# Performance work log

Measured on AMD Instinct MI355X. Metric: run time of the kernel, lower is better.

The kernel has to match this reference:

```python
import jax, jax.numpy as jnp
import numpy as np

D, H, NL, DFF, VS, VT = 512, 8, 6, 2048, 32000, 32000
B, SS, ST = 4, 512, 512
PAD = 1
EPS = 1e-5


def _pos_encoding(S, d):
    pos = jnp.arange(S, dtype=jnp.float32)[:, None]
    div = jnp.exp(jnp.arange(0, d, 2, dtype=jnp.float32) * (-jnp.log(jnp.float32(10000.0)) / d))
    pe = jnp.zeros((S, d), dtype=jnp.float32)
    pe = pe.at[:, 0::2].set(jnp.sin(pos * div))
    pe = pe.at[:, 1::2].set(jnp.cos(pos * div))
    return pe


def _ln(x, g, b):
    m = jnp.mean(x, axis=-1, keepdims=True)
    v = jnp.mean(jnp.square(x - m), axis=-1, keepdims=True)
    return (x - m) * jax.lax.rsqrt(v + EPS) * g + b


def _mha(q, k, v, Wq, Wk, Wv, Wo, mask):
    # q,k,v: [B,S,D]; W*: [D,D] (torch Linear: y = x @ W.T); mask True -> masked
    Bq, Sq, _ = q.shape
    Sk = k.shape[1]
    dk = D // H
    Q = (q @ Wq.T).reshape(Bq, Sq, H, dk).transpose(0, 2, 1, 3)
    K = (k @ Wk.T).reshape(Bq, Sk, H, dk).transpose(0, 2, 1, 3)
    V = (v @ Wv.T).reshape(Bq, Sk, H, dk).transpose(0, 2, 1, 3)
    scores = jnp.einsum('bhqd,bhkd->bhqk', Q, K) / jnp.sqrt(jnp.float32(dk))
    scores = jnp.where(mask, -jnp.inf, scores)
    w = jax.nn.softmax(scores, axis=-1)
    w = jnp.nan_to_num(w)  # matches torch.nan_to_num after softmax of all -inf rows
    out = jnp.einsum('bhqk,bhkd->bhqd', w, V)
    out = out.transpose(0, 2, 1, 3).reshape(Bq, Sq, D)
    return out @ Wo.T


def _ffn(x, w1, b1, w2, b2):
    return jax.nn.relu(x @ w1.T + b1) @ w2.T + b2


def setup_inputs() -> dict:
    key = jax.random.key(0)
    ks = jax.random.split(key, 48)
    i = iter(range(48))
    n = lambda shape, s=0.02: jax.random.normal(ks[next(i)], shape, dtype=jnp.float32) * s
    inp = {
        'src': jax.random.randint(ks[next(i)], (B, SS), 0, VS),
        'tgt': jax.random.randint(ks[next(i)], (B, ST), 0, VT),
        'src_embed': n((VS, D)),
        'tgt_embed': n((VT, D)),
        'enc_Wq': n((NL, D, D)), 'enc_Wk': n((NL, D, D)), 'enc_Wv': n((NL, D, D)), 'enc_Wo': n((NL, D, D)),
        'enc_w1': n((NL, DFF, D)), 'enc_b1': jnp.zeros((NL, DFF)),
        'enc_w2': n((NL, D, DFF)), 'enc_b2': jnp.zeros((NL, D)),
        'enc_ln1g': jnp.ones((NL, D)), 'enc_ln1b': jnp.zeros((NL, D)),
        'enc_ln2g': jnp.ones((NL, D)), 'enc_ln2b': jnp.zeros((NL, D)),
        'enc_lnfg': jnp.ones((D,)), 'enc_lnfb': jnp.zeros((D,)),
        'dec_sWq': n((NL, D, D)), 'dec_sWk': n((NL, D, D)), 'dec_sWv': n((NL, D, D)), 'dec_sWo': n((NL, D, D)),
        'dec_cWq': n((NL, D, D)), 'dec_cWk': n((NL, D, D)), 'dec_cWv': n((NL, D, D)), 'dec_cWo': n((NL, D, D)),
        'dec_w1': n((NL, DFF, D)), 'dec_b1': jnp.zeros((NL, DFF)),
        'dec_w2': n((NL, D, DFF)), 'dec_b2': jnp.zeros((NL, D)),
        'dec_ln1g': jnp.ones((NL, D)), 'dec_ln1b': jnp.zeros((NL, D)),
        'dec_ln2g': jnp.ones((NL, D)), 'dec_ln2b': jnp.zeros((NL, D)),
        'dec_ln3g': jnp.ones((NL, D)), 'dec_ln3b': jnp.zeros((NL, D)),
        'dec_lnfg': jnp.ones((D,)), 'dec_lnfb': jnp.zeros((D,)),
        'out_W': n((VT, D)), 'out_b': jnp.zeros((VT,)),
    }
    return inp


def reference(src, tgt, src_embed, tgt_embed,
              enc_Wq, enc_Wk, enc_Wv, enc_Wo, enc_w1, enc_b1, enc_w2, enc_b2,
              enc_ln1g, enc_ln1b, enc_ln2g, enc_ln2b, enc_lnfg, enc_lnfb,
              dec_sWq, dec_sWk, dec_sWv, dec_sWo, dec_cWq, dec_cWk, dec_cWv, dec_cWo,
              dec_w1, dec_b1, dec_w2, dec_b2,
              dec_ln1g, dec_ln1b, dec_ln2g, dec_ln2b, dec_ln3g, dec_ln3b,
              dec_lnfg, dec_lnfb, out_W, out_b):
    scale = jnp.sqrt(jnp.float32(D))
    src_mask = (src == PAD)[:, None, None, :]                      # [B,1,1,SS]
    causal = jnp.triu(jnp.ones((ST, ST), dtype=bool), k=1)[None, None]
    tgt_mask = (tgt == PAD)[:, None, None, :] | causal             # [B,1,ST,ST]

    # Encoder
    x = src_embed[src] * scale + _pos_encoding(SS, D)[None]
    for l in range(NL):
        nrm = _ln(x, enc_ln1g[l], enc_ln1b[l])
        x = x + _mha(nrm, nrm, nrm, enc_Wq[l], enc_Wk[l], enc_Wv[l], enc_Wo[l], src_mask)
        x = x + _ffn(_ln(x, enc_ln2g[l], enc_ln2b[l]), enc_w1[l], enc_b1[l], enc_w2[l], enc_b2[l])
    memory = _ln(x, enc_lnfg, enc_lnfb)

    # Decoder
    y = tgt_embed[tgt] * scale + _pos_encoding(ST, D)[None]
    for l in range(NL):
        nrm = _ln(y, dec_ln1g[l], dec_ln1b[l])
        y = y + _mha(nrm, nrm, nrm, dec_sWq[l], dec_sWk[l], dec_sWv[l], dec_sWo[l], tgt_mask)
        nrm = _ln(y, dec_ln2g[l], dec_ln2b[l])
        y = y + _mha(nrm, memory, memory, dec_cWq[l], dec_cWk[l], dec_cWv[l], dec_cWo[l], src_mask)
        y = y + _ffn(_ln(y, dec_ln3g[l], dec_ln3b[l]), dec_w1[l], dec_b1[l], dec_w2[l], dec_b2[l])
    y = _ln(y, dec_lnfg, dec_lnfb)

    logits = y @ out_W.T + out_b                                   # [B,ST,VT]
    return logits
```

## Files before the change

kernel.cpp:

```cpp
#include <hip/hip_runtime.h>
#include <hip/hip_bf16.h>
#include <math.h>

#define Dm    512
#define Hh    8
#define NLay  6
#define DFFm  2048
#define Bb    4
#define NTOK  2048
#define PADID 1
#define LNEPS 1e-5f
#define S2W   262144

typedef __attribute__((ext_vector_type(8))) short short8;
typedef __attribute__((ext_vector_type(4))) float f32x4;
typedef unsigned short u16;

__device__ __forceinline__ u16 f2bf(float f) {
    union { float f; unsigned int i; } x; x.f = f;
    unsigned int r = x.i + 0x7fffu + ((x.i >> 16) & 1u);
    return (u16)(r >> 16);
}

typedef const __attribute__((address_space(1))) void* as1cv;
typedef __attribute__((address_space(3))) void* as3v;
__device__ __forceinline__ void gl_lds16(const u16* g, u16* l) {
    __builtin_amdgcn_global_load_lds((as1cv)g, (as3v)l, 16, 0, 0);
}

#define SYNC_VM(N) do { \
    asm volatile("s_waitcnt vmcnt(" #N ")" ::: "memory"); \
    __builtin_amdgcn_s_barrier(); \
    __builtin_amdgcn_sched_barrier(0); \
} while (0)

__device__ __forceinline__ void swz_tile(int& mt, int& nt) {
    const int nwg  = gridDim.x * gridDim.y;
    const int orig = blockIdx.y * gridDim.x + blockIdx.x;
    const int q8 = nwg >> 3, r8 = nwg & 7;
    const int xcd = orig & 7, idx = orig >> 3;
    const int wgid = (xcd < r8 ? xcd * (q8 + 1) : r8 * (q8 + 1) + (xcd - r8) * q8) + idx;
    const int MT = gridDim.y;
    mt = wgid % MT;
    nt = wgid / MT;
}

struct CvtJobs {
    const float* s[17];
    u16*         d[17];
    long         n4[17];
};
__global__ __launch_bounds__(256) void cvt_many(CvtJobs j) {
    const int job = blockIdx.y;
    const long n4 = j.n4[job];
    const float* in = j.s[job];
    u16* out = j.d[job];
    long i = (long)blockIdx.x * 256 + threadIdx.x;
    const long stride = (long)gridDim.x * 256;
    for (; i < n4; i += stride) {
        float4 v = ((const float4*)in)[i];
        ushort4 o;
        o.x = f2bf(v.x); o.y = f2bf(v.y); o.z = f2bf(v.z); o.w = f2bf(v.w);
        ((ushort4*)out)[i] = o;
    }
}

__global__ __launch_bounds__(256) void gemm_bt(
    const u16* __restrict__ A0, const u16* __restrict__ A1,
    const u16* __restrict__ A2, int lda,
    const u16* __restrict__ B0, const u16* __restrict__ B1,
    const u16* __restrict__ B2, int ldb,
    float* Cf, u16* Cb, int csm,
    const float* __restrict__ bias, int relu,
    int Kc, int ns, int vth, int koff, u16* vtp)
{
    __shared__ u16 As[2][4096];
    __shared__ u16 Bs[2][4096];
    int mt, nt; swz_tile(mt, nt);
    const int m0 = mt << 6, n0 = nt << 6;
    const int t = threadIdx.x, lane = t & 63, wave = t >> 6;
    const int wr = (wave >> 1) << 5, wc = (wave & 1) << 5;
    const int fr = lane & 15, fq = lane >> 4;
    const int srow = t >> 3;
    const int sch  = (t & 7) ^ (srow & 7);

    const int p = n0 >> 9;
    const u16* Amat = (p == 0) ? A0 : (p == 1 ? A1 : A2);
    const u16* Bmat; int nb;
    if (B1) { Bmat = (p == 0) ? B0 : (p == 1 ? B1 : B2); nb = n0 & 511; }
    else    { Bmat = B0; nb = n0; }
    const long kb = (long)blockIdx.z * Kc;

    const u16* Ag0 = Amat + (long)(m0 + srow) * lda + kb + (sch << 3);
    const u16* Ag1 = Ag0 + 32L * lda;
    const u16* Bg0 = Bmat + (long)(nb + srow) * ldb + kb + (sch << 3);
    const u16* Bg1 = Bg0 + 32L * ldb;

    f32x4 acc[2][2];
    #pragma unroll
    for (int i = 0; i < 2; i++)
        #pragma unroll
        for (int j = 0; j < 2; j++) acc[i][j] = (f32x4){0.f, 0.f, 0.f, 0.f};

    const int nk = Kc >> 6;
    gl_lds16(Ag0, &As[0][t << 3]);
    gl_lds16(Ag1, &As[0][(t + 256) << 3]);
    gl_lds16(Bg0, &Bs[0][t << 3]);
    gl_lds16(Bg1, &Bs[0][(t + 256) << 3]);
    __syncthreads();
    for (int ki = 0; ki < nk; ki++) {
        const int cur = ki & 1;
        if (ki + 1 < nk) {
            const int ko = (ki + 1) << 6;
            gl_lds16(Ag0 + ko, &As[cur ^ 1][t << 3]);
            gl_lds16(Ag1 + ko, &As[cur ^ 1][(t + 256) << 3]);
            gl_lds16(Bg0 + ko, &Bs[cur ^ 1][t << 3]);
            gl_lds16(Bg1 + ko, &Bs[cur ^ 1][(t + 256) << 3]);
        }
        const int r0 = wr + fr, r1 = wr + 16 + fr;
        const int c0 = wc + fr, c1 = wc + 16 + fr;
        #pragma unroll
        for (int h = 0; h < 2; h++) {
            const int lc = fq | (h << 2);
            short8 af0 = *(const short8*)&As[cur][(r0 << 6) + ((lc ^ (r0 & 7)) << 3)];
            short8 af1 = *(const short8*)&As[cur][(r1 << 6) + ((lc ^ (r1 & 7)) << 3)];
            short8 bf0 = *(const short8*)&Bs[cur][(c0 << 6) + ((lc ^ (c0 & 7)) << 3)];
            short8 bf1 = *(const short8*)&Bs[cur][(c1 << 6) + ((lc ^ (c1 & 7)) << 3)];
            acc[0][0] = __builtin_amdgcn_mfma_f32_16x16x32_bf16(af0, bf0, acc[0][0], 0, 0, 0);
            acc[0][1] = __builtin_amdgcn_mfma_f32_16x16x32_bf16(af0, bf1, acc[0][1], 0, 0, 0);
            acc[1][0] = __builtin_amdgcn_mfma_f32_16x16x32_bf16(af1, bf0, acc[1][0], 0, 0, 0);
            acc[1][1] = __builtin_amdgcn_mfma_f32_16x16x32_bf16(af1, bf1, acc[1][1], 0, 0, 0);
        }
        __syncthreads();
    }

    #pragma unroll
    for (int i = 0; i < 2; i++) {
        #pragma unroll
        for (int j = 0; j < 2; j++) {
            const int nl  = n0 + wc + (j << 4) + fr;
            const int mlb = m0 + wr + (i << 4) + (fq << 2);
            const float bsv = bias ? bias[nl] : 0.f;
            #pragma unroll
            for (int r = 0; r < 4; r++) {
                const int ml = mlb + r;
                if (ns > 1) {
                    float v = acc[i][j][r] + (blockIdx.z == 0 ? bsv : 0.f);
                    unsafeAtomicAdd(&Cf[(long)ml * csm + nl + koff], v);
                } else {
                    float v = acc[i][j][r] + bsv;
                    if (nl >= vth) {
                        vtp[(long)(ml >> 9) * S2W + (long)(nl - vth) * 512 + (ml & 511)] = f2bf(v);
                    } else {
                        if (relu) v = fmaxf(v, 0.f);
                        long ci = (long)ml * csm + nl + koff;
                        if (Cf) Cf[ci] = v;
                        if (Cb) Cb[ci] = f2bf(v);
                    }
                }
            }
        }
    }
}

__global__ __launch_bounds__(256) void gemm_kv6(
    const u16* __restrict__ A,
    const u16* __restrict__ Wk, const u16* __restrict__ Wv,
    u16* __restrict__ kc, u16* __restrict__ vtc)
{
    __shared__ u16 As[2][4096];
    __shared__ u16 Bs[2][4096];
    int mt, nt; swz_tile(mt, nt);
    const int m0 = mt << 6, n0 = nt << 6;
    const int z = blockIdx.z;
    const int t = threadIdx.x, lane = t & 63, wave = t >> 6;
    const int wr = (wave >> 1) << 5, wc = (wave & 1) << 5;
    const int fr = lane & 15, fq = lane >> 4;
    const int srow = t >> 3;
    const int sch  = (t & 7) ^ (srow & 7);

    const int p = n0 >> 9;
    const u16* Bmat = ((p == 0) ? Wk : Wv) + (size_t)z * S2W;
    const int nb = n0 & 511;

    const u16* Ag0 = A + (long)(m0 + srow) * 512 + (sch << 3);
    const u16* Ag1 = Ag0 + 32L * 512;
    const u16* Bg0 = Bmat + (long)(nb + srow) * 512 + (sch << 3);
    const u16* Bg1 = Bg0 + 32L * 512;

    f32x4 acc[2][2];
    #pragma unroll
    for (int i = 0; i < 2; i++)
        #pragma unroll
        for (int j = 0; j < 2; j++) acc[i][j] = (f32x4){0.f, 0.f, 0.f, 0.f};

    gl_lds16(Ag0, &As[0][t << 3]);
    gl_lds16(Ag1, &As[0][(t + 256) << 3]);
    gl_lds16(Bg0, &Bs[0][t << 3]);
    gl_lds16(Bg1, &Bs[0][(t + 256) << 3]);
    __syncthreads();
    for (int ki = 0; ki < 8; ki++) {
        const int cur = ki & 1;
        if (ki + 1 < 8) {
            const int ko = (ki + 1) << 6;
            gl_lds16(Ag0 + ko, &As[cur ^ 1][t << 3]);
            gl_lds16(Ag1 + ko, &As[cur ^ 1][(t + 256) << 3]);
            gl_lds16(Bg0 + ko, &Bs[cur ^ 1][t << 3]);
            gl_lds16(Bg1 + ko, &Bs[cur ^ 1][(t + 256) << 3]);
        }
        const int r0 = wr + fr, r1 = wr + 16 + fr;
        const int c0 = wc + fr, c1 = wc + 16 + fr;
        #pragma unroll
        for (int h = 0; h < 2; h++) {
            const int lc = fq | (h << 2);
            short8 af0 = *(const short8*)&As[cur][(r0 << 6) + ((lc ^ (r0 & 7)) << 3)];
            short8 af1 = *(const short8*)&As[cur][(r1 << 6) + ((lc ^ (r1 & 7)) << 3)];
            short8 bf0 = *(const short8*)&Bs[cur][(c0 << 6) + ((lc ^ (c0 & 7)) << 3)];
            short8 bf1 = *(const short8*)&Bs[cur][(c1 << 6) + ((lc ^ (c1 & 7)) << 3)];
            acc[0][0] = __builtin_amdgcn_mfma_f32_16x16x32_bf16(af0, bf0, acc[0][0], 0, 0, 0);
            acc[0][1] = __builtin_amdgcn_mfma_f32_16x16x32_bf16(af0, bf1, acc[0][1], 0, 0, 0);
            acc[1][0] = __builtin_amdgcn_mfma_f32_16x16x32_bf16(af1, bf0, acc[1][0], 0, 0, 0);
            acc[1][1] = __builtin_amdgcn_mfma_f32_16x16x32_bf16(af1, bf1, acc[1][1], 0, 0, 0);
        }
        __syncthreads();
    }

    #pragma unroll
    for (int i = 0; i < 2; i++) {
        #pragma unroll
        for (int j = 0; j < 2; j++) {
            const int nl  = n0 + wc + (j << 4) + fr;
            const int mlb = m0 + wr + (i << 4) + (fq << 2);
            #pragma unroll
            for (int r = 0; r < 4; r++) {
                const int ml = mlb + r;
                const u16 v = f2bf(acc[i][j][r]);
                if (nl < 512)
                    kc[(long)z * NTOK * 512 + (long)ml * 512 + nl] = v;
                else
                    vtc[(long)z * Bb * S2W + (long)(ml >> 9) * S2W +
                        (long)(nl - 512) * 512 + (ml & 511)] = v;
            }
        }
    }
}

__global__ __launch_bounds__(256) void gemm_big(
    const u16* __restrict__ A, int lda,
    const u16* __restrict__ B, int ldb,
    float* Cf, int ldc,
    const float* __restrict__ bias, int K)
{
    __shared__ u16 As[3][4096];
    __shared__ u16 Bs[3][4096];
    int mt, nt; swz_tile(mt, nt);
    const int m0 = mt << 7, n0 = nt << 7;
    const int t = threadIdx.x, lane = t & 63, wave = t >> 6;
    const int wr = (wave >> 1) << 6, wc = (wave & 1) << 6;
    const int fr = lane & 15, fq = lane >> 4;
    const int srow = t >> 2;
    const int sch  = (t & 3) ^ ((srow >> 1) & 3);
    const u16* Ag0 = A + (long)(m0 + srow) * lda + (sch << 3);
    const u16* Ag1 = A + (long)(m0 + 64 + srow) * lda + (sch << 3);
    const u16* Bg0 = B + (long)(n0 + srow) * ldb + (sch << 3);
    const u16* Bg1 = B + (long)(n0 + 64 + srow) * ldb + (sch << 3);

    f32x4 acc[4][4];
    #pragma unroll
    for (int i = 0; i < 4; i++)
        #pragma unroll
        for (int j = 0; j < 4; j++) acc[i][j] = (f32x4){0.f, 0.f, 0.f, 0.f};

    const int nk = K >> 5;
    auto stage = [&](int ki, int buf) {
        const int ko = ki << 5;
        gl_lds16(Ag0 + ko, &As[buf][t << 3]);
        gl_lds16(Ag1 + ko, &As[buf][(t + 256) << 3]);
        gl_lds16(Bg0 + ko, &Bs[buf][t << 3]);
        gl_lds16(Bg1 + ko, &Bs[buf][(t + 256) << 3]);
    };
    stage(0, 0);
    if (nk > 1) { stage(1, 1); SYNC_VM(4); }
    else        { SYNC_VM(0); }

    int cur = 0;
    for (int ki = 0; ki < nk; ki++) {
        const bool st = (ki + 2 < nk);
        if (st) stage(ki + 2, cur == 0 ? 2 : cur - 1);
        short8 af[4], bf[4];
        #pragma unroll
        for (int i = 0; i < 4; i++) {
            const int r = wr + (i << 4) + fr;
            af[i] = *(const short8*)&As[cur][(r << 5) + ((fq ^ ((r >> 1) & 3)) << 3)];
        }
        #pragma unroll
        for (int j = 0; j < 4; j++) {
            const int c = wc + (j << 4) + fr;
            bf[j] = *(const short8*)&Bs[cur][(c << 5) + ((fq ^ ((c >> 1) & 3)) << 3)];
        }
        #pragma unroll
        for (int i = 0; i < 4; i++)
            #pragma unroll
            for (int j = 0; j < 4; j++)
                acc[i][j] = __builtin_amdgcn_mfma_f32_16x16x32_bf16(af[i], bf[j], acc[i][j], 0, 0, 0);
        if (ki + 1 < nk) {
            if (st) SYNC_VM(4);
            else    SYNC_VM(0);
        }
        cur = (cur == 2) ? 0 : cur + 1;
    }

    #pragma unroll
    for (int i = 0; i < 4; i++) {
        #pragma unroll
        for (int j = 0; j < 4; j++) {
            const int nl  = n0 + wc + (j << 4) + fr;
            const int mlb = m0 + wr + (i << 4) + (fq << 2);
            const float bsv = bias ? bias[nl] : 0.f;
            #pragma unroll
            for (int r = 0; r < 4; r++)
                Cf[(long)(mlb + r) * ldc + nl] = acc[i][j][r] + bsv;
        }
    }
}

__global__ __launch_bounds__(256) void attn_fused(
    const u16* __restrict__ qkb, const u16* __restrict__ kb_, int ldk,
    const u16* __restrict__ vt,
    const int* __restrict__ ids, u16* __restrict__ attc, int causal)
{
    __shared__ u16 Ks[2][4096];
    __shared__ u16 Vs[2][4096];
    __shared__ short Ps[4][16][72];
    const int t = threadIdx.x, lane = t & 63, w = t >> 6;
    const int fr = lane & 15, fq = lane >> 4;
    const int qh = w & 1, kvh = w >> 1;
    const int q0 = blockIdx.x << 5, h = blockIdx.y, b = blockIdx.z;

    const u16* qp = qkb + (long)(b * 512 + q0 + (qh << 4) + fr) * 1024 + h * 64 + (fq << 3);
    short8 aq0 = *(const short8*)qp;
    short8 aq1 = *(const short8*)(qp + 32);

    const int sr = t >> 3, sc = (t & 7) ^ (sr & 7);
    const u16* kg0 = kb_ + (long)(b * 512 + sr) * ldk + h * 64 + (sc << 3);
    const u16* kg1 = kg0 + 32L * ldk;
    const u16* vg0 = vt + (long)b * S2W + (long)(h * 64 + sr) * 512 + (sc << 3);
    const u16* vg1 = vg0 + 32L * 512;

    unsigned pmask = 0;
    #pragma unroll
    for (int kt = 0; kt < 8; kt++)
        #pragma unroll
        for (int j = 0; j < 4; j++)
            if (ids[b * 512 + (kt << 6) + (j << 4) + fr] == PADID)
                pmask |= 1u << ((kt << 2) + j);

    const int nkt = causal ? (((q0 + 31) >> 6) + 1) : 8;
    const int nA = (nkt + 1) >> 1, nB = nkt - nA;
    const int myn = kvh ? nB : nA;

    float m[4], l[4]; f32x4 oc[4];
    #pragma unroll
    for (int r = 0; r < 4; r++) { m[r] = -INFINITY; l[r] = 0.f; oc[r] = (f32x4){0.f,0.f,0.f,0.f}; }

    for (int i = 0; i < nA; i++) {
        {
            const long soA = (long)(i << 6);
            gl_lds16(kg0 + soA * ldk, &Ks[0][t << 3]);
            gl_lds16(kg1 + soA * ldk, &Ks[0][(t + 256) << 3]);
            gl_lds16(vg0 + soA,       &Vs[0][t << 3]);
            gl_lds16(vg1 + soA,       &Vs[0][(t + 256) << 3]);
            if (i < nB) {
                const long soB = (long)((nA + i) << 6);
                gl_lds16(kg0 + soB * ldk, &Ks[1][t << 3]);
                gl_lds16(kg1 + soB * ldk, &Ks[1][(t + 256) << 3]);
                gl_lds16(vg0 + soB,       &Vs[1][t << 3]);
                gl_lds16(vg1 + soB,       &Vs[1][(t + 256) << 3]);
            }
        }
        __syncthreads();

        if (i < myn) {
            const int kt = (kvh ? nA : 0) + i;
            f32x4 sc4[4];
            #pragma unroll
            for (int j = 0; j < 4; j++) sc4[j] = (f32x4){0.f,0.f,0.f,0.f};
            #pragma unroll
            for (int j = 0; j < 4; j++) {
                const int rr = (j << 4) + fr;
                short8 bk0 = *(const short8*)&Ks[kvh][rr * 64 + ((fq ^ (rr & 7)) << 3)];
                short8 bk1 = *(const short8*)&Ks[kvh][rr * 64 + (((fq | 4) ^ (rr & 7)) << 3)];
                sc4[j] = __builtin_amdgcn_mfma_f32_16x16x32_bf16(aq0, bk0, sc4[j], 0, 0, 0);
                sc4[j] = __builtin_amdgcn_mfma_f32_16x16x32_bf16(aq1, bk1, sc4[j], 0, 0, 0);
            }
            const int s0 = kt << 6;
            #pragma unroll
            for (int r = 0; r < 4; r++) {
                const int qa = q0 + (qh << 4) + (fq << 2) + r;
                float mx = -INFINITY;
                #pragma unroll
                for (int j = 0; j < 4; j++) {
                    bool msk = ((pmask >> ((kt << 2) + j)) & 1) ||
                               (causal && (s0 + (j << 4) + fr) > qa);
                    float sv = msk ? -INFINITY : sc4[j][r] * 0.125f;
                    sc4[j][r] = sv;
                    mx = fmaxf(mx, sv);
                }
                mx = fmaxf(mx, __shfl_xor(mx, 1)); mx = fmaxf(mx, __shfl_xor(mx, 2));
                mx = fmaxf(mx, __shfl_xor(mx, 4)); mx = fmaxf(mx, __shfl_xor(mx, 8));
                float mnew  = fmaxf(m[r], mx);
                float scale = (mnew == -INFINITY) ? 1.f : __expf(m[r] - mnew);
                float ps = 0.f;
                #pragma unroll
                for (int j = 0; j < 4; j++) {
                    float p2 = (sc4[j][r] == -INFINITY) ? 0.f : __expf(sc4[j][r] - mnew);
                    sc4[j][r] = p2; ps += p2;
                }
                ps += __shfl_xor(ps, 1); ps += __shfl_xor(ps, 2);
                ps += __shfl_xor(ps, 4); ps += __shfl_xor(ps, 8);
                l[r] = l[r] * scale + ps;
                m[r] = mnew;
                #pragma unroll
                for (int j2 = 0; j2 < 4; j2++) oc[j2][r] *= scale;
            }
            #pragma unroll
            for (int r = 0; r < 4; r++)
                #pragma unroll
                for (int j = 0; j < 4; j++)
                    Ps[w][(fq << 2) + r][(j << 4) + fr] = (short)f2bf(sc4[j][r]);
            #pragma unroll
            for (int kc2 = 0; kc2 < 2; kc2++) {
                short8 pa = *(const short8*)&Ps[w][fr][(kc2 << 5) + (fq << 3)];
                #pragma unroll
                for (int j2 = 0; j2 < 4; j2++) {
                    const int rd = (j2 << 4) + fr;
                    const int cch = (((kc2 << 2) | fq) ^ (rd & 7));
                    short8 bv = *(const short8*)&Vs[kvh][rd * 64 + (cch << 3)];
                    oc[j2] = __builtin_amdgcn_mfma_f32_16x16x32_bf16(pa, bv, oc[j2], 0, 0, 0);
                }
            }
        }
        __syncthreads();
    }

    float* Ob = (float*)&Ks[0][0];
    float* Ml = (float*)&Vs[0][0];
    if (kvh == 1) {
        #pragma unroll
        for (int r = 0; r < 4; r++) {
            const int row = (qh << 4) + (fq << 2) + r;
            Ml[(row << 1)]     = m[r];
            Ml[(row << 1) + 1] = l[r];
            #pragma unroll
            for (int j2 = 0; j2 < 4; j2++)
                Ob[(row << 6) + (j2 << 4) + fr] = oc[j2][r];
        }
    }
    __syncthreads();
    if (kvh == 0) {
        #pragma unroll
        for (int r = 0; r < 4; r++) {
            const int row = (qh << 4) + (fq << 2) + r;
            const float mB = Ml[(row << 1)], lB = Ml[(row << 1) + 1];
            const float mN = fmaxf(m[r], mB);
            float sA, sB;
            if (mN == -INFINITY) { sA = 0.f; sB = 0.f; }
            else {
                sA = (m[r] == -INFINITY) ? 0.f : __expf(m[r] - mN);
                sB = (mB   == -INFINITY) ? 0.f : __expf(mB   - mN);
            }
            const float L = l[r] * sA + lB * sB;
            const float inv = (L > 0.f) ? 1.f / L : 0.f;
            #pragma unroll
            for (int j2 = 0; j2 < 4; j2++) {
                float val = (oc[j2][r] * sA + Ob[(row << 6) + (j2 << 4) + fr] * sB) * inv;
                attc[(long)(b * 512 + q0 + (qh << 4) + (fq << 2) + r) * 512 +
                     h * 64 + (j2 << 4) + fr] = f2bf(val);
            }
        }
    }
}

__global__ __launch_bounds__(256) void ln_rows(
    const float* __restrict__ x, const float* __restrict__ g,
    const float* __restrict__ b, u16* __restrict__ out)
{
    int row  = blockIdx.x * 4 + (threadIdx.x >> 6);
    int lane = threadIdx.x & 63;
    const float* xr = x + (long)row * Dm;
    float v[8]; float s = 0.f;
    #pragma unroll
    for (int i = 0; i < 8; i++) { v[i] = xr[lane + (i << 6)]; s += v[i]; }
    #pragma unroll
    for (int o = 32; o > 0; o >>= 1) s += __shfl_xor(s, o);
    float mean = s * (1.f / 512.f);
    float q = 0.f;
    #pragma unroll
    for (int i = 0; i < 8; i++) { float d = v[i] - mean; q += d * d; }
    #pragma unroll
    for (int o = 32; o > 0; o >>= 1) q += __shfl_xor(q, o);
    float rinv = rsqrtf(q * (1.f / 512.f) + LNEPS);
    u16* orow = out + (long)row * Dm;
    #pragma unroll
    for (int i = 0; i < 8; i++) {
        int c = lane + (i << 6);
        orow[c] = f2bf((v[i] - mean) * rinv * g[c] + b[c]);
    }
}

__global__ __launch_bounds__(256) void embed_pe(
    const int* __restrict__ ids, const float* __restrict__ emb,
    float* __restrict__ out)
{
    int idx = blockIdx.x * 256 + threadIdx.x;
    int d   = idx & 511;
    int tok = idx >> 9;
    int s   = tok & 511;
    int id  = ids[tok];
    float val = emb[(long)id * Dm + d] * 22.62741699796952f;
    int i2 = d >> 1;
    float dv  = expf((float)(i2 << 1) * (-9.210340371976184f / 512.f));
    float ang = (float)s * dv;
    val += (d & 1) ? cosf(ang) : sinf(ang);
    out[idx] = val;
}

extern "C" void kernel_launch(void* const* d_in, const int* in_sizes, int n_in,
                              void* d_out, int out_size, void* d_ws, size_t ws_size,
                              hipStream_t stream)
{
    (void)in_sizes; (void)n_in; (void)out_size; (void)ws_size;
    const int*   src       = (const int*)d_in[0];
    const int*   tgt       = (const int*)d_in[1];
    const float* src_embed = (const float*)d_in[2];
    const float* tgt_embed = (const float*)d_in[3];
    const float* enc_b1  = (const float*)d_in[9];
    const float* enc_b2  = (const float*)d_in[11];
    const float* enc_ln1g = (const float*)d_in[12];
    const float* enc_ln1b = (const float*)d_in[13];
    const float* enc_ln2g = (const float*)d_in[14];
    const float* enc_ln2b = (const float*)d_in[15];
    const float* enc_lnfg = (const float*)d_in[16];
    const float* enc_lnfb = (const float*)d_in[17];
    const float* dec_b1  = (const float*)d_in[27];
    const float* dec_b2  = (const float*)d_in[29];
    const float* dec_ln1g = (const float*)d_in[30];
    const float* dec_ln1b = (const float*)d_in[31];
    const float* dec_ln2g = (const float*)d_in[32];
    const float* dec_ln2b = (const float*)d_in[33];
    const float* dec_ln3g = (const float*)d_in[34];
    const float* dec_ln3b = (const float*)d_in[35];
    const float* dec_lnfg = (const float*)d_in[36];
    const float* dec_lnfb = (const float*)d_in[37];
    const float* out_b  = (const float*)d_in[39];

    char* wp = (char*)d_ws;
    auto carve = [&](size_t nbytes) {
        void* p = (void*)wp; wp += (nbytes + 255) & ~(size_t)255; return p;
    };

    const long nW = (long)NLay * S2W;
    const long nF = (long)NLay * DFFm * Dm;
    const long nO = 32000L * Dm;

    u16* Wb[12];
    for (int i = 0; i < 12; i++) Wb[i] = (u16*)carve((size_t)nW * 2);
    u16* w1E  = (u16*)carve((size_t)nF * 2);
    u16* w2E  = (u16*)carve((size_t)nF * 2);
    u16* w1D  = (u16*)carve((size_t)nF * 2);
    u16* w2D  = (u16*)carve((size_t)nF * 2);
    u16* outW = (u16*)carve((size_t)nO * 2);

    float* x  = (float*)carve((size_t)NTOK * Dm * 4);
    float* y  = (float*)carve((size_t)NTOK * Dm * 4);
    u16* nrm  = (u16*)carve((size_t)NTOK * Dm * 2);
    u16* qkb  = (u16*)carve((size_t)NTOK * 1024 * 2);
    u16* vt   = (u16*)carve((size_t)Bb * Dm * 512 * 2);
    u16* attc = (u16*)carve((size_t)NTOK * Dm * 2);
    u16* h1   = (u16*)carve((size_t)NTOK * DFFm * 2);
    u16* memn = (u16*)carve((size_t)NTOK * Dm * 2);
    u16* kc6  = (u16*)carve((size_t)NLay * NTOK * 512 * 2);
    u16* vt6  = (u16*)carve((size_t)NLay * Bb * S2W * 2);

    const int wi[12] = {4, 5, 6, 7, 18, 19, 20, 21, 22, 23, 24, 25};
    CvtJobs jobs;
    for (int i = 0; i < 12; i++) {
        jobs.s[i] = (const float*)d_in[wi[i]]; jobs.d[i] = Wb[i]; jobs.n4[i] = nW >> 2;
    }
    jobs.s[12] = (const float*)d_in[8];  jobs.d[12] = w1E;  jobs.n4[12] = nF >> 2;
    jobs.s[13] = (const float*)d_in[10]; jobs.d[13] = w2E;  jobs.n4[13] = nF >> 2;
    jobs.s[14] = (const float*)d_in[26]; jobs.d[14] = w1D;  jobs.n4[14] = nF >> 2;
    jobs.s[15] = (const float*)d_in[28]; jobs.d[15] = w2D;  jobs.n4[15] = nF >> 2;
    jobs.s[16] = (const float*)d_in[38]; jobs.d[16] = outW; jobs.n4[16] = nO >> 2;
    cvt_many<<<dim3(512, 17), 256, 0, stream>>>(jobs);

    const int BIG = 1 << 28;
    u16 *eWq = Wb[0], *eWk = Wb[1], *eWv = Wb[2], *eWo = Wb[3];
    u16 *sWq = Wb[4], *sWk = Wb[5], *sWv = Wb[6], *sWo = Wb[7];
    u16 *cWq = Wb[8], *cWk = Wb[9], *cWv = Wb[10], *cWo = Wb[11];

    embed_pe<<<4096, 256, 0, stream>>>(src, src_embed, x);
    for (int l = 0; l < NLay; l++) {
        const size_t wo = (size_t)l * S2W;
        ln_rows<<<512, 256, 0, stream>>>(x, enc_ln1g + l * Dm, enc_ln1b + l * Dm, nrm);
        gemm_bt<<<dim3(24, 32, 1), 256, 0, stream>>>(nrm, nrm, nrm, 512,
            eWq + wo, eWk + wo, eWv + wo, 512,
            nullptr, qkb, 1024, nullptr, 0, 512, 1, 1024, 0, vt);
        attn_fused<<<dim3(16, Hh, Bb), 256, 0, stream>>>(qkb, qkb + 512, 1024, vt, src, attc, 0);
        gemm_bt<<<dim3(8, 32, 2), 256, 0, stream>>>(attc, attc, attc, 512,
            eWo + wo, nullptr, nullptr, 512,
            x, nullptr, 512, nullptr, 0, 256, 2, BIG, 0, nullptr);
        ln_rows<<<512, 256, 0, stream>>>(x, enc_ln2g + l * Dm, enc_ln2b + l * Dm, nrm);
        gemm_bt<<<dim3(32, 32, 1), 256, 0, stream>>>(nrm, nrm, nrm, 512,
            w1E + (size_t)l * DFFm * Dm, nullptr, nullptr, 512,
            nullptr, h1, DFFm, enc_b1 + l * DFFm, 1, 512, 1, BIG, 0, nullptr);
        gemm_bt<<<dim3(8, 32, 4), 256, 0, stream>>>(h1, h1, h1, DFFm,
            w2E + (size_t)l * Dm * DFFm, nullptr, nullptr, DFFm,
            x, nullptr, 512, enc_b2 + l * Dm, 0, 512, 4, BIG, 0, nullptr);
    }
    ln_rows<<<512, 256, 0, stream>>>(x, enc_lnfg, enc_lnfb, memn);
    gemm_kv6<<<dim3(16, 32, NLay), 256, 0, stream>>>(memn, cWk, cWv, kc6, vt6);

    embed_pe<<<4096, 256, 0, stream>>>(tgt, tgt_embed, y);
    for (int l = 0; l < NLay; l++) {
        const size_t wo = (size_t)l * S2W;
        ln_rows<<<512, 256, 0, stream>>>(y, dec_ln1g + l * Dm, dec_ln1b + l * Dm, nrm);
        gemm_bt<<<dim3(24, 32, 1), 256, 0, stream>>>(nrm, nrm, nrm, 512,
            sWq + wo, sWk + wo, sWv + wo, 512,
            nullptr, qkb, 1024, nullptr, 0, 512, 1, 1024, 0, vt);
        attn_fused<<<dim3(16, Hh, Bb), 256, 0, stream>>>(qkb, qkb + 512, 1024, vt, tgt, attc, 1);
        gemm_bt<<<dim3(8, 32, 2), 256, 0, stream>>>(attc, attc, attc, 512,
            sWo + wo, nullptr, nullptr, 512,
            y, nullptr, 512, nullptr, 0, 256, 2, BIG, 0, nullptr);
        ln_rows<<<512, 256, 0, stream>>>(y, dec_ln2g + l * Dm, dec_ln2b + l * Dm, nrm);
        gemm_bt<<<dim3(8, 32, 1), 256, 0, stream>>>(nrm, nrm, nrm, 512,
            cWq + wo, nullptr, nullptr, 512,
            nullptr, qkb, 1024, nullptr, 0, 512, 1, BIG, 0, nullptr);
        attn_fused<<<dim3(16, Hh, Bb), 256, 0, stream>>>(qkb,
            kc6 + (size_t)l * NTOK * 512, 512, vt6 + (size_t)l * Bb * S2W, src, attc, 0);
        gemm_bt<<<dim3(8, 32, 2), 256, 0, stream>>>(attc, attc, attc, 512,
            cWo + wo, nullptr, nullptr, 512,
            y, nullptr, 512, nullptr, 0, 256, 2, BIG, 0, nullptr);
        ln_rows<<<512, 256, 0, stream>>>(y, dec_ln3g + l * Dm, dec_ln3b + l * Dm, nrm);
        gemm_bt<<<dim3(32, 32, 1), 256, 0, stream>>>(nrm, nrm, nrm, 512,
            w1D + (size_t)l * DFFm * Dm, nullptr, nullptr, 512,
            nullptr, h1, DFFm, dec_b1 + l * DFFm, 1, 512, 1, BIG, 0, nullptr);
        gemm_bt<<<dim3(8, 32, 4), 256, 0, stream>>>(h1, h1, h1, DFFm,
            w2D + (size_t)l * Dm * DFFm, nullptr, nullptr, DFFm,
            y, nullptr, 512, dec_b2 + l * Dm, 0, 512, 4, BIG, 0, nullptr);
    }
    ln_rows<<<512, 256, 0, stream>>>(y, dec_lnfg, dec_lnfb, nrm);

    gemm_big<<<dim3(250, 16), 256, 0, stream>>>(nrm, 512, outW, 512,
        (float*)d_out, 32000, out_b, 512);
}
```

Before: 1.570 ms.

## Switch GEMM mainloops to 3-stage LDS pipeline with 32-wide K tiles

Both bf16 GEMM kernels now use three LDS buffers of 64x32 tiles instead of two 64x64 buffers. Loads are issued two K-steps ahead, and synchronisation uses a vmcnt-based wait (SYNC_VM) in place of a full barrier after every step. The swizzle is adapted to 4 chunks per row. The goal is to hide global-load latency better and use less LDS per block, in exchange for twice as many loop iterations and syncs with fewer MFMAs each.

Result: slower. 1.650 ms (+5.1%).

```diff
diff --git a/kernel.cpp b/kernel.cpp
--- a/kernel.cpp
+++ b/kernel.cpp
@@ -74,15 +74,15 @@
     const float* __restrict__ bias, int relu,
     int Kc, int ns, int vth, int koff, u16* vtp)
 {
-    __shared__ u16 As[2][4096];
-    __shared__ u16 Bs[2][4096];
+    __shared__ u16 As[3][2048];
+    __shared__ u16 Bs[3][2048];
     int mt, nt; swz_tile(mt, nt);
     const int m0 = mt << 6, n0 = nt << 6;
     const int t = threadIdx.x, lane = t & 63, wave = t >> 6;
     const int wr = (wave >> 1) << 5, wc = (wave & 1) << 5;
     const int fr = lane & 15, fq = lane >> 4;
-    const int srow = t >> 3;
-    const int sch  = (t & 7) ^ (srow & 7);
+    const int srow = t >> 2;
+    const int sch  = (t & 3) ^ ((srow >> 1) & 3);
 
     const int p = n0 >> 9;
     const u16* Amat = (p == 0) ? A0 : (p == 1 ? A1 : A2);
@@ -91,10 +91,8 @@
     else    { Bmat = B0; nb = n0; }
     const long kb = (long)blockIdx.z * Kc;
 
-    const u16* Ag0 = Amat + (long)(m0 + srow) * lda + kb + (sch << 3);
-    const u16* Ag1 = Ag0 + 32L * lda;
-    const u16* Bg0 = Bmat + (long)(nb + srow) * ldb + kb + (sch << 3);
-    const u16* Bg1 = Bg0 + 32L * ldb;
+    const u16* Ag = Amat + (long)(m0 + srow) * lda + kb + (sch << 3);
+    const u16* Bg = Bmat + (long)(nb + srow) * ldb + kb + (sch << 3);
 
     f32x4 acc[2][2];
     #pragma unroll
@@ -102,36 +100,35 @@
         #pragma unroll
         for (int j = 0; j < 2; j++) acc[i][j] = (f32x4){0.f, 0.f, 0.f, 0.f};
 
-    const int nk = Kc >> 6;
-    gl_lds16(Ag0, &As[0][t << 3]);
-    gl_lds16(Ag1, &As[0][(t + 256) << 3]);
-    gl_lds16(Bg0, &Bs[0][t << 3]);
-    gl_lds16(Bg1, &Bs[0][(t + 256) << 3]);
-    __syncthreads();
+    const int nk = Kc >> 5;
+    auto stage = [&](int ki, int buf) {
+        const int ko = ki << 5;
+        gl_lds16(Ag + ko, &As[buf][t << 3]);
+        gl_lds16(Bg + ko, &Bs[buf][t << 3]);
+    };
+    stage(0, 0);
+    if (nk > 1) { stage(1, 1); SYNC_VM(2); }
+    else        { SYNC_VM(0); }
+
+    int cur = 0;
     for (int ki = 0; ki < nk; ki++) {
-        const int cur = ki & 1;
-        if (ki + 1 < nk) {
-            const int ko = (ki + 1) << 6;
-            gl_lds16(Ag0 + ko, &As[cur ^ 1][t << 3]);
-            gl_lds16(Ag1 + ko, &As[cur ^ 1][(t + 256) << 3]);
-            gl_lds16(Bg0 + ko, &Bs[cur ^ 1][t << 3]);
-            gl_lds16(Bg1 + ko, &Bs[cur ^ 1][(t + 256) << 3]);
-        }
+        const bool st = (ki + 2 < nk);
+        if (st) stage(ki + 2, cur == 0 ? 2 : cur - 1);
         const int r0 = wr + fr, r1 = wr + 16 + fr;
         const int c0 = wc + fr, c1 = wc + 16 + fr;
-        #pragma unroll
-        for (int h = 0; h < 2; h++) {
-            const int lc = fq | (h << 2);
-            short8 af0 = *(const short8*)&As[cur][(r0 << 6) + ((lc ^ (r0 & 7)) << 3)];
-            short8 af1 = *(const short8*)&As[cur][(r1 << 6) + ((lc ^ (r1 & 7)) << 3)];
-            short8 bf0 = *(const short8*)&Bs[cur][(c0 << 6) + ((lc ^ (c0 & 7)) << 3)];
-            short8 bf1 = *(const short8*)&Bs[cur][(c1 << 6) + ((lc ^ (c1 & 7)) << 3)];
-            acc[0][0] = __builtin_amdgcn_mfma_f32_16x16x32_bf16(af0, bf0, acc[0][0], 0, 0, 0);
-            acc[0][1] = __builtin_amdgcn_mfma_f32_16x16x32_bf16(af0, bf1, acc[0][1], 0, 0, 0);
-            acc[1][0] = __builtin_amdgcn_mfma_f32_16x16x32_bf16(af1, bf0, acc[1][0], 0, 0, 0);
-            acc[1][1] = __builtin_amdgcn_mfma_f32_16x16x32_bf16(af1, bf1, acc[1][1], 0, 0, 0);
-        }
-        __syncthreads();
+        short8 af0 = *(const short8*)&As[cur][(r0 << 5) + ((fq ^ ((r0 >> 1) & 3)) << 3)];
+        short8 af1 = *(const short8*)&As[cur][(r1 << 5) + ((fq ^ ((r1 >> 1) & 3)) << 3)];
+        short8 bf0 = *(const short8*)&Bs[cur][(c0 << 5) + ((fq ^ ((c0 >> 1) & 3)) << 3)];
+        short8 bf1 = *(const short8*)&Bs[cur][(c1 << 5) + ((fq ^ ((c1 >> 1) & 3)) << 3)];
+        acc[0][0] = __builtin_amdgcn_mfma_f32_16x16x32_bf16(af0, bf0, acc[0][0], 0, 0, 0);
+        acc[0][1] = __builtin_amdgcn_mfma_f32_16x16x32_bf16(af0, bf1, acc[0][1], 0, 0, 0);
+        acc[1][0] = __builtin_amdgcn_mfma_f32_16x16x32_bf16(af1, bf0, acc[1][0], 0, 0, 0);
+        acc[1][1] = __builtin_amdgcn_mfma_f32_16x16x32_bf16(af1, bf1, acc[1][1], 0, 0, 0);
+        if (ki + 1 < nk) {
+            if (st) SYNC_VM(2);
+            else    SYNC_VM(0);
+        }
+        cur = (cur == 2) ? 0 : cur + 1;
     }
 
     #pragma unroll
@@ -168,25 +165,23 @@
     const u16* __restrict__ Wk, const u16* __restrict__ Wv,
     u16* __restrict__ kc, u16* __restrict__ vtc)
 {
-    __shared__ u16 As[2][4096];
-    __shared__ u16 Bs[2][4096];
+    __shared__ u16 As[3][2048];
+    __shared__ u16 Bs[3][2048];
     int mt, nt; swz_tile(mt, nt);
     const int m0 = mt << 6, n0 = nt << 6;
     const int z = blockIdx.z;
     const int t = threadIdx.x, lane = t & 63, wave = t >> 6;
     const int wr = (wave >> 1) << 5, wc = (wave & 1) << 5;
     const int fr = lane & 15, fq = lane >> 4;
-    const int srow = t >> 3;
-    const int sch  = (t & 7) ^ (srow & 7);
+    const int srow = t >> 2;
+    const int sch  = (t & 3) ^ ((srow >> 1) & 3);
 
     const int p = n0 >> 9;
     const u16* Bmat = ((p == 0) ? Wk : Wv) + (size_t)z * S2W;
     const int nb = n0 & 511;
 
-    const u16* Ag0 = A + (long)(m0 + srow) * 512 + (sch << 3);
-    const u16* Ag1 = Ag0 + 32L * 512;
-    const u16* Bg0 = Bmat + (long)(nb + srow) * 512 + (sch << 3);
-    const u16* Bg1 = Bg0 + 32L * 512;
+    const u16* Ag = A + (long)(m0 + srow) * 512 + (sch << 3);
+    const u16* Bg = Bmat + (long)(nb + srow) * 512 + (sch << 3);
 
     f32x4 acc[2][2];
     #pragma unroll
@@ -194,35 +189,34 @@
         #pragma unroll
         for (int j = 0; j < 2; j++) acc[i][j] = (f32x4){0.f, 0.f, 0.f, 0.f};
 
-    gl_lds16(Ag0, &As[0][t << 3]);
-    gl_lds16(Ag1, &As[0][(t + 256) << 3]);
-    gl_lds16(Bg0, &Bs[0][t << 3]);
-    gl_lds16(Bg1, &Bs[0][(t + 256) << 3]);
-    __syncthreads();
-    for (int ki = 0; ki < 8; ki++) {
-        const int cur = ki & 1;
-        if (ki + 1 < 8) {
-            const int ko = (ki + 1) << 6;
-            gl_lds16(Ag0 + ko, &As[cur ^ 1][t << 3]);
-            gl_lds16(Ag1 + ko, &As[cur ^ 1][(t + 256) << 3]);
-            gl_lds16(Bg0 + ko, &Bs[cur ^ 1][t << 3]);
-            gl_lds16(Bg1 + ko, &Bs[cur ^ 1][(t + 256) << 3]);
-        }
+    auto stage = [&](int ki, int buf) {
+        const int ko = ki << 5;
+        gl_lds16(Ag + ko, &As[buf][t << 3]);
+        gl_lds16(Bg + ko, &Bs[buf][t << 3]);
+    };
+    stage(0, 0);
+    stage(1, 1);
+    SYNC_VM(2);
+
+    int cur = 0;
+    for (int ki = 0; ki < 16; ki++) {
+        const bool st = (ki + 2 < 16);
+        if (st) stage(ki + 2, cur == 0 ? 2 : cur - 1);
         const int r0 = wr + fr, r1 = wr + 16 + fr;
         const int c0 = wc + fr, c1 = wc + 16 + fr;
-        #pragma unroll
-        for (int h = 0; h < 2; h++) {
-            const int lc = fq | (h << 2);
-            short8 af0 = *(const short8*)&As[cur][(r0 << 6) + ((lc ^ (r0 & 7)) << 3)];
-            short8 af1 = *(const short8*)&As[cur][(r1 << 6) + ((lc ^ (r1 & 7)) << 3)];
-            short8 bf0 = *(const short8*)&Bs[cur][(c0 << 6) + ((lc ^ (c0 & 7)) << 3)];
-            short8 bf1 = *(const short8*)&Bs[cur][(c1 << 6) + ((lc ^ (c1 & 7)) << 3)];
-            acc[0][0] = __builtin_amdgcn_mfma_f32_16x16x32_bf16(af0, bf0, acc[0][0], 0, 0, 0);
-            acc[0][1] = __builtin_amdgcn_mfma_f32_16x16x32_bf16(af0, bf1, acc[0][1], 0, 0, 0);
-            acc[1][0] = __builtin_amdgcn_mfma_f32_16x16x32_bf16(af1, bf0, acc[1][0], 0, 0, 0);
-            acc[1][1] = __builtin_amdgcn_mfma_f32_16x16x32_bf16(af1, bf1, acc[1][1], 0, 0, 0);
-        }
-        __syncthreads();
+        short8 af0 = *(const short8*)&As[cur][(r0 << 5) + ((fq ^ ((r0 >> 1) & 3)) << 3)];
+        short8 af1 = *(const short8*)&As[cur][(r1 << 5) + ((fq ^ ((r1 >> 1) & 3)) << 3)];
+        short8 bf0 = *(const short8*)&Bs[cur][(c0 << 5) + ((fq ^ ((c0 >> 1) & 3)) << 3)];
+        short8 bf1 = *(const short8*)&Bs[cur][(c1 << 5) + ((fq ^ ((c1 >> 1) & 3)) << 3)];
+        acc[0][0] = __builtin_amdgcn_mfma_f32_16x16x32_bf16(af0, bf0, acc[0][0], 0, 0, 0);
+        acc[0][1] = __builtin_amdgcn_mfma_f32_16x16x32_bf16(af0, bf1, acc[0][1], 0, 0, 0);
+        acc[1][0] = __builtin_amdgcn_mfma_f32_16x16x32_bf16(af1, bf0, acc[1][0], 0, 0, 0);
+        acc[1][1] = __builtin_amdgcn_mfma_f32_16x16x32_bf16(af1, bf1, acc[1][1], 0, 0, 0);
+        if (ki + 1 < 16) {
+            if (st) SYNC_VM(2);
+            else    SYNC_VM(0);
+        }
+        cur = (cur == 2) ? 0 : cur + 1;
     }
 
     #pragma unroll
```
